# Kernel tuning notes

Hardware: AMD Instinct MI355X
Metric: run time of the kernel (lower is better)

## Reference

```python
import jax, jax.numpy as jnp
import numpy as np
from functools import partial


def _lstm_cell(x, h, c, Wk, Wr, b):
    # keras LSTMCell: gates packed as [i, f, g(candidate), o]
    z = x @ Wk + h @ Wr + b  # [B, 4U]
    i, f, g, o = jnp.split(z, 4, axis=-1)
    i = jax.nn.sigmoid(i)
    f = jax.nn.sigmoid(f)
    g = jnp.tanh(g)
    o = jax.nn.sigmoid(o)
    c_new = f * c + i * g
    h_new = o * jnp.tanh(c_new)
    return h_new, c_new


def setup_inputs() -> dict:
    key = jax.random.key(0)
    B, T, F, U, S = 1024, 128, 128, 512, 96
    k1, k2, k3, k4 = jax.random.split(key, 4)
    s = 0.05
    return {
        "inputs": jax.random.normal(k1, (B, T, F), dtype=jnp.float32),
        "Wk": jax.random.normal(k2, (F, 4 * U), dtype=jnp.float32) * s,
        "Wr": jax.random.normal(k3, (U, 4 * U), dtype=jnp.float32) * s,
        "b": jnp.zeros((4 * U,), dtype=jnp.float32),
        "Wd": jax.random.normal(k4, (U, F), dtype=jnp.float32) * s,
        "bd": jnp.zeros((F,), dtype=jnp.float32),
        "output_steps": S,
    }


def reference(inputs, Wk, Wr, b, Wd, bd, output_steps):
    B = inputs.shape[0]
    U = Wr.shape[0]
    h0 = jnp.zeros((B, U), dtype=inputs.dtype)
    c0 = jnp.zeros((B, U), dtype=inputs.dtype)

    # warmup: run RNN over the input sequence, keep final state
    def warm_step(carry, x_t):
        h, c = carry
        h, c = _lstm_cell(x_t, h, c, Wk, Wr, b)
        return (h, c), None

    (h, c), _ = jax.lax.scan(warm_step, (h0, c0), jnp.swapaxes(inputs, 0, 1))
    pred = h @ Wd + bd  # first prediction [B, F]

    def dec_step(carry, _):
        p, h, c = carry
        h, c = _lstm_cell(p, h, c, Wk, Wr, b)
        p = h @ Wd + bd
        return (p, h, c), p

    _, preds = jax.lax.scan(dec_step, (pred, h, c), None, length=output_steps - 1)
    out = jnp.concatenate([pred[None], preds], axis=0)  # [S, B, F]
    return jnp.swapaxes(out, 0, 1)  # [B, S, F]
```

## Files before the change

### kernel.cpp

```cpp
#include <hip/hip_runtime.h>
#include <hip/hip_bf16.h>

typedef float f32x4 __attribute__((ext_vector_type(4)));
typedef short s16x8 __attribute__((ext_vector_type(8)));
typedef float floatx4 __attribute__((ext_vector_type(4)));

#define DEV static __device__ __forceinline__
#define WAITVM(N) asm volatile("s_waitcnt vmcnt(" #N ")" ::: "memory")

DEV void barrier_pipe() {
  __builtin_amdgcn_sched_barrier(0);
  __builtin_amdgcn_s_barrier();
  __builtin_amdgcn_sched_barrier(0);
}

DEV void gld_lds16(const void* g, void* l) {
  __builtin_amdgcn_global_load_lds(
      (const __attribute__((address_space(1))) void*)g,
      (__attribute__((address_space(3))) void*)l, 16, 0, 0);
}

DEV short f2bf(float x) {
  union { __hip_bfloat16 h; short s; } u;
  u.h = __float2bfloat16(x);
  return u.s;
}

DEV float bf2f(short s) {
  union { unsigned u; float f; } v;
  v.u = ((unsigned)(unsigned short)s) << 16;
  return v.f;
}

DEV void split2(float x, short& hi, short& lo) {
  hi = f2bf(x);
  lo = f2bf(x - bf2f(hi));
}

DEV float sigf(float x) {
  return 1.0f / (1.0f + exp2f(x * -1.44269504f));
}

DEV float tanhf2(float x) {
  float e = exp2f(fmaxf(x, -18.0f) * -2.88539008f);
  return (1.0f - e) / (1.0f + e);
}

DEV void mfma16(f32x4& d, s16x8 a, s16x8 b) {
  asm("v_mfma_f32_16x16x32_bf16 %0, %1, %2, %0" : "+v"(d) : "v"(a), "v"(b));
}

__global__ __launch_bounds__(256)
void prep_w2(const float* __restrict__ Wk, const float* __restrict__ Wr,
             short* __restrict__ WT2) {
  __shared__ float t[64 * 65];
  const int k0 = blockIdx.x * 64, n0 = blockIdx.y * 64;
  const int c = threadIdx.x & 63, r4 = threadIdx.x >> 6;
#pragma unroll
  for (int i = 0; i < 16; ++i) {
    int r = r4 * 16 + i;
    int k = k0 + r, n = n0 + c;
    t[r * 65 + c] = (k < 128) ? Wk[(size_t)k * 2048 + n] : Wr[(size_t)(k - 128) * 2048 + n];
  }
  __syncthreads();
#pragma unroll
  for (int i = 0; i < 16; ++i) {
    int nn = r4 * 16 + i;
    float v = t[c * 65 + nn];
    short hi, lo; split2(v, hi, lo);
    WT2[(size_t)(n0 + nn) * 1280 + k0 + c] = hi;
    WT2[(size_t)(n0 + nn) * 1280 + 640 + k0 + c] = lo;
  }
}

__global__ __launch_bounds__(256)
void wdec_split(const float* __restrict__ Wd, const float* __restrict__ Wk,
                const float* __restrict__ Wr, short* __restrict__ WdecAll) {
  const int n = blockIdx.x * 256 + threadIdx.x;
  const int kp = blockIdx.y;
  float acc = Wr[(size_t)kp * 2048 + n];
#pragma unroll 8
  for (int j = 0; j < 128; ++j)
    acc = fmaf(Wd[(size_t)kp * 128 + j], Wk[(size_t)j * 2048 + n], acc);
  short hi, lo; split2(acc, hi, lo);
  WdecAll[(size_t)n * 1024 + kp] = hi;
  WdecAll[(size_t)n * 1024 + 512 + kp] = lo;
}

__global__ __launch_bounds__(256)
void wd_append(const float* __restrict__ Wd, short* __restrict__ WdecAll) {
  const int t = blockIdx.x * 256 + threadIdx.x;
  const int k = t >> 7, n = t & 127;
  float v = Wd[(size_t)k * 128 + n];
  short hi, lo; split2(v, hi, lo);
  WdecAll[(size_t)(2048 + n) * 1024 + k] = hi;
  WdecAll[(size_t)(2048 + n) * 1024 + 512 + k] = lo;
}

__global__ __launch_bounds__(256)
void bdec_all(const float* __restrict__ bd, const float* __restrict__ Wk,
              const float* __restrict__ b, float* __restrict__ bdecAll) {
  const int n = blockIdx.x * 256 + threadIdx.x;
  if (n < 2048) {
    float acc = b[n];
#pragma unroll 8
    for (int j = 0; j < 128; ++j) acc = fmaf(bd[j], Wk[(size_t)j * 2048 + n], acc);
    bdecAll[n] = acc;
  } else if (n < 2176) {
    bdecAll[n] = bd[n - 2048];
  }
}

__global__ __launch_bounds__(256)
void x0_init(const float* __restrict__ inputs, short* __restrict__ AW0) {
  const int t = blockIdx.x * 256 + threadIdx.x;
  const int r = t >> 4, c0 = (t & 15) * 8;
  const float* src = inputs + (size_t)r * 16384 + c0;
  floatx4 a = *(const floatx4*)src;
  floatx4 b = *(const floatx4*)(src + 4);
  s16x8 vh, vl;
#pragma unroll
  for (int e = 0; e < 8; ++e) {
    float x = (e < 4) ? a[e] : b[e - 4];
    short hi, lo; split2(x, hi, lo);
    vh[e] = hi; vl[e] = lo;
  }
  *(s16x8*)(AW0 + (size_t)r * 1280 + c0) = vh;
  *(s16x8*)(AW0 + (size_t)r * 1280 + 640 + c0) = vl;
}

template <int MODE>
__global__ __launch_bounds__(256)
void lstm_step(const short* __restrict__ Abuf,
               short* __restrict__ hout, int hstride, int hioff, int looff,
               const float* __restrict__ xnext,
               float* __restrict__ Cst,
               const short* __restrict__ W2,
               const float* __restrict__ bias,
               float* __restrict__ out, int sidx, int S) {
  constexpr int NKT = (MODE == 0) ? 20 : 16;
  constexpr int KP  = (MODE == 0) ? 1280 : 1024;
  __shared__ char lds[73728];
  const int tid = threadIdx.x;
  const int lane = tid & 63;
  const int wid = tid >> 6;
  const int wm = wid & 1, wu = wid >> 1;
  const int bid = blockIdx.x;

  bool is16;
  int m0, u0;
  if (MODE == 2) {
    is16 = true; m0 = bid * 64; u0 = 0;
  } else if (MODE == 1 && bid >= 256) {
    is16 = true; m0 = (bid - 256) * 64; u0 = 0;
  } else {
    is16 = false;
    const int jb = bid >> 3;
    const int strip = (bid & 7) + ((jb >> 4) << 3);
    m0 = (jb & 15) * 64;
    u0 = strip * 32;
  }
  const int wbase = (tid & 192) * 16;

  auto stage = [&](int kt, int bsel) {
    char* B = lds + 24576 + bsel * 16384;
#pragma unroll
    for (int p = 0; p < 4; ++p) {
      int idx = p * 256 + tid;
      int r = idx >> 3, jp = idx & 7;
      int j = jp ^ (r & 7);
      int gu = is16 ? (2048 + r) : (((r >> 5) << 9) + u0 + (r & 31));
      gld_lds16(W2 + (size_t)gu * KP + kt * 64 + j * 8, B + p * 4096 + wbase);
    }
    char* A = lds + bsel * 8192;
#pragma unroll
    for (int p = 0; p < 2; ++p) {
      int idx = p * 256 + tid;
      int r = idx >> 3, jp = idx & 7;
      int j = jp ^ (r & 7);
      gld_lds16(Abuf + (size_t)(m0 + r) * KP + kt * 64 + j * 8, A + p * 4096 + wbase);
    }
  };

  f32x4 acc[2][4] = {};
  stage(0, 0);
  stage(1, 1);
#pragma unroll
  for (int kt = 0; kt < NKT; ++kt) {
    if (kt <= NKT - 2) WAITVM(6);
    else WAITVM(0);
    barrier_pipe();
    if (kt + 2 < NKT) stage(kt + 2, (kt + 2) % 3);
    const char* A = lds + (kt % 3) * 8192;
    const char* B = lds + 24576 + (kt % 3) * 16384;
#pragma unroll
    for (int s2 = 0; s2 < 2; ++s2) {
      const int jd = s2 * 4 + (lane >> 4);
      s16x8 av[2], bv[4];
#pragma unroll
      for (int mi = 0; mi < 2; ++mi) {
        int r = wm * 32 + mi * 16 + (lane & 15);
        av[mi] = *(const s16x8*)(A + r * 128 + ((jd ^ (r & 7)) << 4));
      }
#pragma unroll
      for (int g = 0; g < 4; ++g) {
        int rB = g * 32 + wu * 16 + (lane & 15);
        bv[g] = *(const s16x8*)(B + rB * 128 + ((jd ^ (rB & 7)) << 4));
      }
#pragma unroll
      for (int mi = 0; mi < 2; ++mi)
#pragma unroll
        for (int g = 0; g < 4; ++g) mfma16(acc[mi][g], av[mi], bv[g]);
    }
  }

  asm volatile("s_nop 7\ns_nop 7\ns_nop 7");

  if (MODE == 2 || (MODE == 1 && is16)) {
#pragma unroll
    for (int g = 0; g < 4; ++g) {
      const int n = g * 32 + wu * 16 + (lane & 15);
      const float bb = bias[2048 + n];
#pragma unroll
      for (int mi = 0; mi < 2; ++mi) {
#pragma unroll
        for (int rr = 0; rr < 4; ++rr) {
          const int m = m0 + wm * 32 + mi * 16 + ((lane >> 4) << 2) + rr;
          out[(size_t)m * ((size_t)S * 128) + (size_t)sidx * 128 + n] =
              acc[mi][g][rr] + bb;
        }
      }
    }
    return;
  }

  const int u = u0 + wu * 16 + (lane & 15);
  const float bi = bias[u], bf_ = bias[512 + u], bg = bias[1024 + u], bo = bias[1536 + u];
#pragma unroll
  for (int mi = 0; mi < 2; ++mi) {
#pragma unroll
    for (int rr = 0; rr < 4; ++rr) {
      const int m = m0 + wm * 32 + mi * 16 + ((lane >> 4) << 2) + rr;
      const size_t off = (size_t)m * 512 + u;
      float ig = sigf(acc[mi][0][rr] + bi);
      float fg = sigf(acc[mi][1][rr] + bf_);
      float gg = tanhf2(acc[mi][2][rr] + bg);
      float og = sigf(acc[mi][3][rr] + bo);
      float cn = fg * Cst[off] + ig * gg;
      Cst[off] = cn;
      float hv = og * tanhf2(cn);
      short hh, hl; split2(hv, hh, hl);
      hout[(size_t)m * hstride + hioff + u] = hh;
      hout[(size_t)m * hstride + looff + u] = hl;
    }
  }

  if (MODE == 0 && xnext != nullptr && u0 == 0) {
    const int r = tid >> 2;
    const int c0 = (tid & 3) * 32;
    const float* src = xnext + (size_t)(m0 + r) * 16384 + c0;
    short* dst = hout + (size_t)(m0 + r) * hstride;
#pragma unroll
    for (int j = 0; j < 32; j += 8) {
      floatx4 a = *(const floatx4*)(src + j);
      floatx4 b = *(const floatx4*)(src + j + 4);
      s16x8 vh, vl;
#pragma unroll
      for (int e = 0; e < 8; ++e) {
        float x = (e < 4) ? a[e] : b[e - 4];
        short hi, lo; split2(x, hi, lo);
        vh[e] = hi; vl[e] = lo;
      }
      *(s16x8*)(dst + c0 + j) = vh;
      *(s16x8*)(dst + 640 + c0 + j) = vl;
    }
  }
}

extern "C" void kernel_launch(void* const* d_in, const int* in_sizes, int n_in,
                              void* d_out, int out_size, void* d_ws, size_t ws_size,
                              hipStream_t stream) {
  const float* inputs = (const float*)d_in[0];
  const float* Wk = (const float*)d_in[1];
  const float* Wr = (const float*)d_in[2];
  const float* bias = (const float*)d_in[3];
  const float* Wd = (const float*)d_in[4];
  const float* bd = (const float*)d_in[5];
  float* out = (float*)d_out;
  const int S = out_size / (1024 * 128);

  char* w = (char*)d_ws;
  short* WT2     = (short*)w; w += (size_t)2048 * 1280 * 2;
  short* WdecAll = (short*)w; w += (size_t)2176 * 1024 * 2;
  float* bdecA   = (float*)w; w += (size_t)2176 * 4;
  short* AW0 = (short*)w; w += (size_t)1024 * 1280 * 2;
  short* AW1 = (short*)w; w += (size_t)1024 * 1280 * 2;
  short* AD0 = (short*)w; w += (size_t)1024 * 1024 * 2;
  short* AD1 = (short*)w; w += (size_t)1024 * 1024 * 2;
  float* Cst = (float*)w; w += (size_t)1024 * 512 * 4;
  if ((size_t)(w - (char*)d_ws) > ws_size) return;

  hipMemsetAsync(AW0, 0, (size_t)1024 * 1280 * 2, stream);
  hipMemsetAsync(Cst, 0, (size_t)1024 * 512 * 4, stream);

  prep_w2<<<dim3(10, 32), 256, 0, stream>>>(Wk, Wr, WT2);
  wdec_split<<<dim3(8, 512), 256, 0, stream>>>(Wd, Wk, Wr, WdecAll);
  wd_append<<<256, 256, 0, stream>>>(Wd, WdecAll);
  bdec_all<<<9, 256, 0, stream>>>(bd, Wk, bias, bdecA);
  x0_init<<<64, 256, 0, stream>>>(inputs, AW0);

  short* AW[2] = { AW0, AW1 };
  short* AD[2] = { AD0, AD1 };

  for (int t = 0; t < 127; ++t) {
    lstm_step<0><<<256, 256, 0, stream>>>(
        AW[t & 1], AW[(t + 1) & 1], 1280, 128, 768,
        inputs + (size_t)(t + 1) * 128, Cst, WT2, bias, nullptr, 0, S);
  }
  lstm_step<0><<<256, 256, 0, stream>>>(
      AW[1], AD[0], 1024, 0, 512, nullptr, Cst, WT2, bias, nullptr, 0, S);

  for (int s = 1; s < S; ++s) {
    lstm_step<1><<<272, 256, 0, stream>>>(
        AD[(s - 1) & 1], AD[s & 1], 1024, 0, 512, nullptr, Cst,
        WdecAll, bdecA, out, s - 1, S);
  }
  lstm_step<2><<<16, 256, 0, stream>>>(
      AD[(S - 1) & 1], nullptr, 0, 0, 0, nullptr, Cst,
      WdecAll, bdecA, out, S - 1, S);
}
```

Measured before the change: 2.891 ms.

## Fuse all LSTM timesteps into one persistent kernel with a grid barrier

Replaces the roughly 224 per-timestep kernel launches with a single persistent kernel of 272 blocks. Blocks synchronise between steps through an atomic counter and a generation flag in global memory. The decode phase now reads h from the warmup buffer layout, which removes the separate AD buffers. The aim is to cut launch overhead and tail gaps between steps. In exchange it adds a spin-barrier cost each step and relies on all 272 blocks being co-resident, otherwise it deadlocks. The step count of 224 is hardcoded, which assumes S is 96.

```diff
diff --git a/kernel.cpp b/kernel.cpp
--- a/kernel.cpp
+++ b/kernel.cpp
@@ -129,151 +129,185 @@
   *(s16x8*)(AW0 + (size_t)r * 1280 + 640 + c0) = vl;
 }
 
-template <int MODE>
-__global__ __launch_bounds__(256)
-void lstm_step(const short* __restrict__ Abuf,
-               short* __restrict__ hout, int hstride, int hioff, int looff,
-               const float* __restrict__ xnext,
-               float* __restrict__ Cst,
-               const short* __restrict__ W2,
-               const float* __restrict__ bias,
-               float* __restrict__ out, int sidx, int S) {
-  constexpr int NKT = (MODE == 0) ? 20 : 16;
-  constexpr int KP  = (MODE == 0) ? 1280 : 1024;
+__global__ __launch_bounds__(256, 2)
+void lstm_persist(const float* __restrict__ inputs,
+                  const short* __restrict__ WT2,
+                  const short* __restrict__ WdecAll,
+                  const float* __restrict__ bias0,
+                  const float* __restrict__ bdecA,
+                  short* __restrict__ AW0, short* __restrict__ AW1,
+                  float* __restrict__ Cst,
+                  float* __restrict__ out, int S,
+                  unsigned* __restrict__ sync) {
   __shared__ char lds[73728];
   const int tid = threadIdx.x;
   const int lane = tid & 63;
   const int wid = tid >> 6;
   const int wm = wid & 1, wu = wid >> 1;
   const int bid = blockIdx.x;
-
-  bool is16;
+  const bool is16 = (bid >= 256);
   int m0, u0;
-  if (MODE == 2) {
-    is16 = true; m0 = bid * 64; u0 = 0;
-  } else if (MODE == 1 && bid >= 256) {
-    is16 = true; m0 = (bid - 256) * 64; u0 = 0;
+  if (is16) {
+    m0 = (bid - 256) * 64; u0 = 0;
   } else {
-    is16 = false;
     const int jb = bid >> 3;
     const int strip = (bid & 7) + ((jb >> 4) << 3);
     m0 = (jb & 15) * 64;
     u0 = strip * 32;
   }
   const int wbase = (tid & 192) * 16;
-
-  auto stage = [&](int kt, int bsel) {
-    char* B = lds + 24576 + bsel * 16384;
-#pragma unroll
-    for (int p = 0; p < 4; ++p) {
-      int idx = p * 256 + tid;
-      int r = idx >> 3, jp = idx & 7;
-      int j = jp ^ (r & 7);
-      int gu = is16 ? (2048 + r) : (((r >> 5) << 9) + u0 + (r & 31));
-      gld_lds16(W2 + (size_t)gu * KP + kt * 64 + j * 8, B + p * 4096 + wbase);
-    }
-    char* A = lds + bsel * 8192;
-#pragma unroll
-    for (int p = 0; p < 2; ++p) {
-      int idx = p * 256 + tid;
-      int r = idx >> 3, jp = idx & 7;
-      int j = jp ^ (r & 7);
-      gld_lds16(Abuf + (size_t)(m0 + r) * KP + kt * 64 + j * 8, A + p * 4096 + wbase);
-    }
-  };
-
-  f32x4 acc[2][4] = {};
-  stage(0, 0);
-  stage(1, 1);
-#pragma unroll
-  for (int kt = 0; kt < NKT; ++kt) {
-    if (kt <= NKT - 2) WAITVM(6);
-    else WAITVM(0);
-    barrier_pipe();
-    if (kt + 2 < NKT) stage(kt + 2, (kt + 2) % 3);
-    const char* A = lds + (kt % 3) * 8192;
-    const char* B = lds + 24576 + (kt % 3) * 16384;
-#pragma unroll
-    for (int s2 = 0; s2 < 2; ++s2) {
-      const int jd = s2 * 4 + (lane >> 4);
-      s16x8 av[2], bv[4];
-#pragma unroll
-      for (int mi = 0; mi < 2; ++mi) {
-        int r = wm * 32 + mi * 16 + (lane & 15);
-        av[mi] = *(const s16x8*)(A + r * 128 + ((jd ^ (r & 7)) << 4));
+  const bool xconv = (!is16 && u0 == 0);
+  unsigned* cnt = sync;
+  unsigned* gen = sync + 32;
+
+  for (int t = 0; t < 224; ++t) {
+    const bool warm = (t < 128);
+    const int s = t - 127;
+    const int nkt = warm ? 20 : 16;
+    const int kp = warm ? 1280 : 1024;
+    const short* W = warm ? WT2 : WdecAll;
+    const float* bs = warm ? bias0 : bdecA;
+    const short* Ain = (t & 1) ? AW1 : AW0;
+    short* hout = ((t + 1) & 1) ? AW1 : AW0;
+    const bool gate_on = !is16 && (warm || s <= 95);
+    const bool active = gate_on || (is16 && !warm);
+
+    if (active) {
+      auto stage = [&](int kt, int bsel) {
+        char* B = lds + 24576 + bsel * 16384;
+#pragma unroll
+        for (int p = 0; p < 4; ++p) {
+          int idx = p * 256 + tid;
+          int r = idx >> 3, jp = idx & 7;
+          int j = jp ^ (r & 7);
+          int gu = is16 ? (2048 + r) : (((r >> 5) << 9) + u0 + (r & 31));
+          gld_lds16(W + (size_t)gu * kp + kt * 64 + j * 8, B + p * 4096 + wbase);
+        }
+        char* A = lds + bsel * 8192;
+        const int ka = warm ? kt * 64
+                            : ((kt < 8) ? (128 + kt * 64) : (768 + (kt - 8) * 64));
+#pragma unroll
+        for (int p = 0; p < 2; ++p) {
+          int idx = p * 256 + tid;
+          int r = idx >> 3, jp = idx & 7;
+          int j = jp ^ (r & 7);
+          gld_lds16(Ain + (size_t)(m0 + r) * 1280 + ka + j * 8, A + p * 4096 + wbase);
+        }
+      };
+
+      f32x4 acc[2][4] = {};
+      stage(0, 0);
+      stage(1, 1);
+      int sl = 0;
+      for (int kt = 0; kt < nkt; ++kt) {
+        if (kt < nkt - 1) WAITVM(6);
+        else WAITVM(0);
+        barrier_pipe();
+        if (kt + 2 < nkt) stage(kt + 2, (sl >= 1) ? sl - 1 : 2);
+        const char* A = lds + sl * 8192;
+        const char* B = lds + 24576 + sl * 16384;
+#pragma unroll
+        for (int s2 = 0; s2 < 2; ++s2) {
+          const int jd = s2 * 4 + (lane >> 4);
+          s16x8 av[2], bv[4];
+#pragma unroll
+          for (int mi = 0; mi < 2; ++mi) {
+            int r = wm * 32 + mi * 16 + (lane & 15);
+            av[mi] = *(const s16x8*)(A + r * 128 + ((jd ^ (r & 7)) << 4));
+          }
+#pragma unroll
+          for (int g = 0; g < 4; ++g) {
+            int rB = g * 32 + wu * 16 + (lane & 15);
+            bv[g] = *(const s16x8*)(B + rB * 128 + ((jd ^ (rB & 7)) << 4));
+          }
+#pragma unroll
+          for (int mi = 0; mi < 2; ++mi)
+#pragma unroll
+            for (int g = 0; g < 4; ++g) mfma16(acc[mi][g], av[mi], bv[g]);
+        }
+        sl = (sl == 2) ? 0 : sl + 1;
       }
-#pragma unroll
-      for (int g = 0; g < 4; ++g) {
-        int rB = g * 32 + wu * 16 + (lane & 15);
-        bv[g] = *(const s16x8*)(B + rB * 128 + ((jd ^ (rB & 7)) << 4));
-      }
-#pragma unroll
-      for (int mi = 0; mi < 2; ++mi)
-#pragma unroll
-        for (int g = 0; g < 4; ++g) mfma16(acc[mi][g], av[mi], bv[g]);
-    }
-  }
-
-  asm volatile("s_nop 7\ns_nop 7\ns_nop 7");
-
-  if (MODE == 2 || (MODE == 1 && is16)) {
-#pragma unroll
-    for (int g = 0; g < 4; ++g) {
-      const int n = g * 32 + wu * 16 + (lane & 15);
-      const float bb = bias[2048 + n];
-#pragma unroll
-      for (int mi = 0; mi < 2; ++mi) {
-#pragma unroll
-        for (int rr = 0; rr < 4; ++rr) {
-          const int m = m0 + wm * 32 + mi * 16 + ((lane >> 4) << 2) + rr;
-          out[(size_t)m * ((size_t)S * 128) + (size_t)sidx * 128 + n] =
-              acc[mi][g][rr] + bb;
+
+      asm volatile("s_nop 7\ns_nop 7\ns_nop 7");
+
+      if (is16) {
+#pragma unroll
+        for (int g = 0; g < 4; ++g) {
+          const int n = g * 32 + wu * 16 + (lane & 15);
+          const float bb = bdecA[2048 + n];
+#pragma unroll
+          for (int mi = 0; mi < 2; ++mi) {
+#pragma unroll
+            for (int rr = 0; rr < 4; ++rr) {
+              const int m = m0 + wm * 32 + mi * 16 + ((lane >> 4) << 2) + rr;
+              out[(size_t)m * ((size_t)S * 128) + (size_t)(s - 1) * 128 + n] =
+                  acc[mi][g][rr] + bb;
+            }
+          }
+        }
+      } else {
+        const int u = u0 + wu * 16 + (lane & 15);
+        const float bi = bs[u], bf_ = bs[512 + u], bg = bs[1024 + u], bo = bs[1536 + u];
+#pragma unroll
+        for (int mi = 0; mi < 2; ++mi) {
+#pragma unroll
+          for (int rr = 0; rr < 4; ++rr) {
+            const int m = m0 + wm * 32 + mi * 16 + ((lane >> 4) << 2) + rr;
+            const size_t off = (size_t)m * 512 + u;
+            float ig = sigf(acc[mi][0][rr] + bi);
+            float fg = sigf(acc[mi][1][rr] + bf_);
+            float gg = tanhf2(acc[mi][2][rr] + bg);
+            float og = sigf(acc[mi][3][rr] + bo);
+            float cn = fg * Cst[off] + ig * gg;
+            Cst[off] = cn;
+            float hv = og * tanhf2(cn);
+            short hh, hl; split2(hv, hh, hl);
+            hout[(size_t)m * 1280 + 128 + u] = hh;
+            hout[(size_t)m * 1280 + 768 + u] = hl;
+          }
+        }
+        if (warm && t < 127 && xconv) {
+          const float* xn = inputs + (size_t)(t + 1) * 128;
+          const int r = tid >> 2;
+          const int c0 = (tid & 3) * 32;
+          const float* src = xn + (size_t)(m0 + r) * 16384 + c0;
+          short* dst = hout + (size_t)(m0 + r) * 1280;
+#pragma unroll
+          for (int j = 0; j < 32; j += 8) {
+            floatx4 a = *(const floatx4*)(src + j);
+            floatx4 b = *(const floatx4*)(src + j + 4);
+            s16x8 vh, vl;
+#pragma unroll
+            for (int e = 0; e < 8; ++e) {
+              float x = (e < 4) ? a[e] : b[e - 4];
+              short hi, lo; split2(x, hi, lo);
+              vh[e] = hi; vl[e] = lo;
+            }
+            *(s16x8*)(dst + c0 + j) = vh;
+            *(s16x8*)(dst + 640 + c0 + j) = vl;
+          }
         }
       }
     }
-    return;
-  }
-
-  const int u = u0 + wu * 16 + (lane & 15);
-  const float bi = bias[u], bf_ = bias[512 + u], bg = bias[1024 + u], bo = bias[1536 + u];
-#pragma unroll
-  for (int mi = 0; mi < 2; ++mi) {
-#pragma unroll
-    for (int rr = 0; rr < 4; ++rr) {
-      const int m = m0 + wm * 32 + mi * 16 + ((lane >> 4) << 2) + rr;
-      const size_t off = (size_t)m * 512 + u;
-      float ig = sigf(acc[mi][0][rr] + bi);
-      float fg = sigf(acc[mi][1][rr] + bf_);
-      float gg = tanhf2(acc[mi][2][rr] + bg);
-      float og = sigf(acc[mi][3][rr] + bo);
-      float cn = fg * Cst[off] + ig * gg;
-      Cst[off] = cn;
-      float hv = og * tanhf2(cn);
-      short hh, hl; split2(hv, hh, hl);
-      hout[(size_t)m * hstride + hioff + u] = hh;
-      hout[(size_t)m * hstride + looff + u] = hl;
+
+    __syncthreads();
+    if (tid == 0) {
+      __threadfence();
+      unsigned a = __hip_atomic_fetch_add(cnt, 1u, __ATOMIC_ACQ_REL,
+                                          __HIP_MEMORY_SCOPE_AGENT);
+      if (a == (unsigned)(272 * (t + 1) - 1)) {
+        __hip_atomic_store(gen, (unsigned)(t + 1), __ATOMIC_RELEASE,
+                           __HIP_MEMORY_SCOPE_AGENT);
+      } else {
+        unsigned g;
+        do {
+          __builtin_amdgcn_s_sleep(8);
+          g = __hip_atomic_load(gen, __ATOMIC_RELAXED, __HIP_MEMORY_SCOPE_AGENT);
+        } while (g < (unsigned)(t + 1));
+      }
+      __threadfence();
     }
-  }
-
-  if (MODE == 0 && xnext != nullptr && u0 == 0) {
-    const int r = tid >> 2;
-    const int c0 = (tid & 3) * 32;
-    const float* src = xnext + (size_t)(m0 + r) * 16384 + c0;
-    short* dst = hout + (size_t)(m0 + r) * hstride;
-#pragma unroll
-    for (int j = 0; j < 32; j += 8) {
-      floatx4 a = *(const floatx4*)(src + j);
-      floatx4 b = *(const floatx4*)(src + j + 4);
-      s16x8 vh, vl;
-#pragma unroll
-      for (int e = 0; e < 8; ++e) {
-        float x = (e < 4) ? a[e] : b[e - 4];
-        short hi, lo; split2(x, hi, lo);
-        vh[e] = hi; vl[e] = lo;
-      }
-      *(s16x8*)(dst + c0 + j) = vh;
-      *(s16x8*)(dst + 640 + c0 + j) = vl;
-    }
+    __syncthreads();
   }
 }
 
@@ -295,13 +329,13 @@
   float* bdecA   = (float*)w; w += (size_t)2176 * 4;
   short* AW0 = (short*)w; w += (size_t)1024 * 1280 * 2;
   short* AW1 = (short*)w; w += (size_t)1024 * 1280 * 2;
-  short* AD0 = (short*)w; w += (size_t)1024 * 1024 * 2;
-  short* AD1 = (short*)w; w += (size_t)1024 * 1024 * 2;
   float* Cst = (float*)w; w += (size_t)1024 * 512 * 4;
+  unsigned* sync = (unsigned*)w; w += 256;
   if ((size_t)(w - (char*)d_ws) > ws_size) return;
 
   hipMemsetAsync(AW0, 0, (size_t)1024 * 1280 * 2, stream);
   hipMemsetAsync(Cst, 0, (size_t)1024 * 512 * 4, stream);
+  hipMemsetAsync(sync, 0, 256, stream);
 
   prep_w2<<<dim3(10, 32), 256, 0, stream>>>(Wk, Wr, WT2);
   wdec_split<<<dim3(8, 512), 256, 0, stream>>>(Wd, Wk, Wr, WdecAll);
@@ -309,23 +343,6 @@
   bdec_all<<<9, 256, 0, stream>>>(bd, Wk, bias, bdecA);
   x0_init<<<64, 256, 0, stream>>>(inputs, AW0);
 
-  short* AW[2] = { AW0, AW1 };
-  short* AD[2] = { AD0, AD1 };
-
-  for (int t = 0; t < 127; ++t) {
-    lstm_step<0><<<256, 256, 0, stream>>>(
-        AW[t & 1], AW[(t + 1) & 1], 1280, 128, 768,
-        inputs + (size_t)(t + 1) * 128, Cst, WT2, bias, nullptr, 0, S);
-  }
-  lstm_step<0><<<256, 256, 0, stream>>>(
-      AW[1], AD[0], 1024, 0, 512, nullptr, Cst, WT2, bias, nullptr, 0, S);
-
-  for (int s = 1; s < S; ++s) {
-    lstm_step<1><<<272, 256, 0, stream>>>(
-        AD[(s - 1) & 1], AD[s & 1], 1024, 0, 512, nullptr, Cst,
-        WdecAll, bdecA, out, s - 1, S);
-  }
-  lstm_step<2><<<16, 256, 0, stream>>>(
-      AD[(S - 1) & 1], nullptr, 0, 0, 0, nullptr, Cst,
-      WdecAll, bdecA, out, S - 1, S);
-}
+  lstm_persist<<<272, 256, 0, stream>>>(inputs, WT2, WdecAll, bias, bdecA,
+                                        AW0, AW1, Cst, out, S, sync);
+}
```

Measured after the change: 7.138 ms. 147% more time.

## Halve LSTM gate tile width to double grid size per step

Applied to the files above, without the earlier changes.

Each recurrent-step block now covers 64 rows by 16 units per gate instead of 32, so the grid grows from 256 to 512 blocks (528 in decode mode). Each wave computes a single 16-row slice with four gate accumulators. The projection path is split into its own branch with eight 16-wide column tiles, and the warmup kernel uses a smaller LDS footprint. The aim is better latency hiding and CU occupancy per timestep. The cost is that every A-tile row is loaded by twice as many blocks, so there is less reuse and more global and L2 traffic.

```diff
diff --git a/kernel.cpp b/kernel.cpp
--- a/kernel.cpp
+++ b/kernel.cpp
@@ -131,121 +131,85 @@
 
 template <int MODE>
 __global__ __launch_bounds__(256)
-void lstm_step(const short* __restrict__ Abuf,
-               short* __restrict__ hout, int hstride, int hioff, int looff,
+void lstm_step(const short* __restrict__ Ain, short* __restrict__ hout,
+               int hstride, int hioff, int looff,
                const float* __restrict__ xnext,
                float* __restrict__ Cst,
                const short* __restrict__ W2,
                const float* __restrict__ bias,
                float* __restrict__ out, int sidx, int S) {
   constexpr int NKT = (MODE == 0) ? 20 : 16;
-  constexpr int KP  = (MODE == 0) ? 1280 : 1024;
-  __shared__ char lds[73728];
-  const int tid = threadIdx.x;
-  const int lane = tid & 63;
-  const int wid = tid >> 6;
-  const int wm = wid & 1, wu = wid >> 1;
+  constexpr int ASTR = (MODE == 0) ? 1280 : 1024;
+  constexpr int LDSZ = (MODE == 0) ? 49152 : 73728;
+  __shared__ char lds[LDSZ];
+  const int tid = threadIdx.x, lane = tid & 63, wid = tid >> 6;
+  const int l15 = lane & 15, l4 = lane >> 4;
   const int bid = blockIdx.x;
-
-  bool is16;
-  int m0, u0;
-  if (MODE == 2) {
-    is16 = true; m0 = bid * 64; u0 = 0;
-  } else if (MODE == 1 && bid >= 256) {
-    is16 = true; m0 = (bid - 256) * 64; u0 = 0;
-  } else {
-    is16 = false;
-    const int jb = bid >> 3;
-    const int strip = (bid & 7) + ((jb >> 4) << 3);
-    m0 = (jb & 15) * 64;
-    u0 = strip * 32;
-  }
   const int wbase = (tid & 192) * 16;
-
-  auto stage = [&](int kt, int bsel) {
-    char* B = lds + 24576 + bsel * 16384;
-#pragma unroll
-    for (int p = 0; p < 4; ++p) {
-      int idx = p * 256 + tid;
-      int r = idx >> 3, jp = idx & 7;
-      int j = jp ^ (r & 7);
-      int gu = is16 ? (2048 + r) : (((r >> 5) << 9) + u0 + (r & 31));
-      gld_lds16(W2 + (size_t)gu * KP + kt * 64 + j * 8, B + p * 4096 + wbase);
-    }
-    char* A = lds + bsel * 8192;
-#pragma unroll
-    for (int p = 0; p < 2; ++p) {
-      int idx = p * 256 + tid;
-      int r = idx >> 3, jp = idx & 7;
-      int j = jp ^ (r & 7);
-      gld_lds16(Abuf + (size_t)(m0 + r) * KP + kt * 64 + j * 8, A + p * 4096 + wbase);
-    }
-  };
-
-  f32x4 acc[2][4] = {};
-  stage(0, 0);
-  stage(1, 1);
-#pragma unroll
-  for (int kt = 0; kt < NKT; ++kt) {
-    if (kt <= NKT - 2) WAITVM(6);
-    else WAITVM(0);
-    barrier_pipe();
-    if (kt + 2 < NKT) stage(kt + 2, (kt + 2) % 3);
-    const char* A = lds + (kt % 3) * 8192;
-    const char* B = lds + 24576 + (kt % 3) * 16384;
-#pragma unroll
-    for (int s2 = 0; s2 < 2; ++s2) {
-      const int jd = s2 * 4 + (lane >> 4);
-      s16x8 av[2], bv[4];
-#pragma unroll
-      for (int mi = 0; mi < 2; ++mi) {
-        int r = wm * 32 + mi * 16 + (lane & 15);
-        av[mi] = *(const s16x8*)(A + r * 128 + ((jd ^ (r & 7)) << 4));
-      }
-#pragma unroll
-      for (int g = 0; g < 4; ++g) {
-        int rB = g * 32 + wu * 16 + (lane & 15);
-        bv[g] = *(const s16x8*)(B + rB * 128 + ((jd ^ (rB & 7)) << 4));
-      }
-#pragma unroll
-      for (int mi = 0; mi < 2; ++mi)
-#pragma unroll
-        for (int g = 0; g < 4; ++g) mfma16(acc[mi][g], av[mi], bv[g]);
-    }
-  }
-
-  asm volatile("s_nop 7\ns_nop 7\ns_nop 7");
-
-  if (MODE == 2 || (MODE == 1 && is16)) {
-#pragma unroll
-    for (int g = 0; g < 4; ++g) {
-      const int n = g * 32 + wu * 16 + (lane & 15);
-      const float bb = bias[2048 + n];
-#pragma unroll
-      for (int mi = 0; mi < 2; ++mi) {
-#pragma unroll
-        for (int rr = 0; rr < 4; ++rr) {
-          const int m = m0 + wm * 32 + mi * 16 + ((lane >> 4) << 2) + rr;
-          out[(size_t)m * ((size_t)S * 128) + (size_t)sidx * 128 + n] =
-              acc[mi][g][rr] + bb;
+  const bool proj = (MODE == 2) || (MODE == 1 && bid >= 512);
+
+  if (!proj) {
+    const int strip = bid & 31;
+    const int mblk = bid >> 5;
+    const int m0 = mblk * 64;
+    const int u0 = strip * 16;
+
+    auto stage = [&](int kt, int bsel) {
+      char* B = lds + 24576 + bsel * 8192;
+#pragma unroll
+      for (int p = 0; p < 2; ++p) {
+        int idx = p * 256 + tid;
+        int r = idx >> 3, jp = idx & 7;
+        int j = jp ^ (r & 7);
+        int gu = ((r >> 4) << 9) + u0 + (r & 15);
+        gld_lds16(W2 + (size_t)gu * ASTR + kt * 64 + j * 8, B + p * 4096 + wbase);
+      }
+      char* A = lds + bsel * 8192;
+#pragma unroll
+      for (int p = 0; p < 2; ++p) {
+        int idx = p * 256 + tid;
+        int r = idx >> 3, jp = idx & 7;
+        int j = jp ^ (r & 7);
+        gld_lds16(Ain + (size_t)(m0 + r) * ASTR + kt * 64 + j * 8, A + p * 4096 + wbase);
+      }
+    };
+
+    f32x4 acc[4] = {};
+    stage(0, 0);
+    stage(1, 1);
+#pragma unroll
+    for (int kt = 0; kt < NKT; ++kt) {
+      if (kt == NKT - 1) { WAITVM(0); } else { WAITVM(4); }
+      barrier_pipe();
+      if (kt + 2 < NKT) stage(kt + 2, (kt + 2) % 3);
+      const char* A = lds + (kt % 3) * 8192;
+      const char* B = lds + 24576 + (kt % 3) * 8192;
+#pragma unroll
+      for (int s2 = 0; s2 < 2; ++s2) {
+        const int jd = s2 * 4 + l4;
+        const int r = wid * 16 + l15;
+        s16x8 av = *(const s16x8*)(A + r * 128 + ((jd ^ (r & 7)) << 4));
+#pragma unroll
+        for (int g = 0; g < 4; ++g) {
+          const int rB = g * 16 + l15;
+          s16x8 bv = *(const s16x8*)(B + rB * 128 + ((jd ^ (rB & 7)) << 4));
+          mfma16(acc[g], av, bv);
         }
       }
     }
-    return;
-  }
-
-  const int u = u0 + wu * 16 + (lane & 15);
-  const float bi = bias[u], bf_ = bias[512 + u], bg = bias[1024 + u], bo = bias[1536 + u];
-#pragma unroll
-  for (int mi = 0; mi < 2; ++mi) {
+
+    asm volatile("s_nop 7\ns_nop 7\ns_nop 7");
+
+    const int u = u0 + l15;
+    const float bi = bias[u], bf_ = bias[512 + u], bg = bias[1024 + u], bo = bias[1536 + u];
 #pragma unroll
     for (int rr = 0; rr < 4; ++rr) {
-      const int m = m0 + wm * 32 + mi * 16 + ((lane >> 4) << 2) + rr;
+      const int m = m0 + wid * 16 + (l4 << 2) + rr;
       const size_t off = (size_t)m * 512 + u;
-      float ig = sigf(acc[mi][0][rr] + bi);
-      float fg = sigf(acc[mi][1][rr] + bf_);
-      float gg = tanhf2(acc[mi][2][rr] + bg);
-      float og = sigf(acc[mi][3][rr] + bo);
+      float ig = sigf(acc[0][rr] + bi);
+      float fg = sigf(acc[1][rr] + bf_);
+      float gg = tanhf2(acc[2][rr] + bg);
+      float og = sigf(acc[3][rr] + bo);
       float cn = fg * Cst[off] + ig * gg;
       Cst[off] = cn;
       float hv = og * tanhf2(cn);
@@ -253,26 +217,85 @@
       hout[(size_t)m * hstride + hioff + u] = hh;
       hout[(size_t)m * hstride + looff + u] = hl;
     }
-  }
-
-  if (MODE == 0 && xnext != nullptr && u0 == 0) {
-    const int r = tid >> 2;
-    const int c0 = (tid & 3) * 32;
-    const float* src = xnext + (size_t)(m0 + r) * 16384 + c0;
-    short* dst = hout + (size_t)(m0 + r) * hstride;
-#pragma unroll
-    for (int j = 0; j < 32; j += 8) {
-      floatx4 a = *(const floatx4*)(src + j);
-      floatx4 b = *(const floatx4*)(src + j + 4);
-      s16x8 vh, vl;
-#pragma unroll
-      for (int e = 0; e < 8; ++e) {
-        float x = (e < 4) ? a[e] : b[e - 4];
-        short hi, lo; split2(x, hi, lo);
-        vh[e] = hi; vl[e] = lo;
-      }
-      *(s16x8*)(dst + c0 + j) = vh;
-      *(s16x8*)(dst + 640 + c0 + j) = vl;
+
+    if (MODE == 0 && xnext != nullptr && strip == 0) {
+      const int r = tid >> 2;
+      const int c0 = (tid & 3) * 32;
+      const float* src = xnext + (size_t)(m0 + r) * 16384 + c0;
+      short* dst = hout + (size_t)(m0 + r) * 1280;
+#pragma unroll
+      for (int j = 0; j < 32; j += 8) {
+        floatx4 a = *(const floatx4*)(src + j);
+        floatx4 b = *(const floatx4*)(src + j + 4);
+        s16x8 vh, vl;
+#pragma unroll
+        for (int e = 0; e < 8; ++e) {
+          float x = (e < 4) ? a[e] : b[e - 4];
+          short hi, lo; split2(x, hi, lo);
+          vh[e] = hi; vl[e] = lo;
+        }
+        *(s16x8*)(dst + c0 + j) = vh;
+        *(s16x8*)(dst + 640 + c0 + j) = vl;
+      }
+    }
+  } else {
+    const int pb = (MODE == 2) ? bid : bid - 512;
+    const int m0 = pb * 64;
+
+    auto stageP = [&](int kt, int bsel) {
+      char* B = lds + 24576 + bsel * 16384;
+#pragma unroll
+      for (int p = 0; p < 4; ++p) {
+        int idx = p * 256 + tid;
+        int r = idx >> 3, jp = idx & 7;
+        int j = jp ^ (r & 7);
+        gld_lds16(W2 + (size_t)(2048 + r) * 1024 + kt * 64 + j * 8, B + p * 4096 + wbase);
+      }
+      char* A = lds + bsel * 8192;
+#pragma unroll
+      for (int p = 0; p < 2; ++p) {
+        int idx = p * 256 + tid;
+        int r = idx >> 3, jp = idx & 7;
+        int j = jp ^ (r & 7);
+        gld_lds16(Ain + (size_t)(m0 + r) * 1024 + kt * 64 + j * 8, A + p * 4096 + wbase);
+      }
+    };
+
+    f32x4 acc[8] = {};
+    stageP(0, 0);
+    stageP(1, 1);
+#pragma unroll
+    for (int kt = 0; kt < 16; ++kt) {
+      if (kt == 15) { WAITVM(0); } else { WAITVM(6); }
+      barrier_pipe();
+      if (kt + 2 < 16) stageP(kt + 2, (kt + 2) % 3);
+      const char* A = lds + (kt % 3) * 8192;
+      const char* B = lds + 24576 + (kt % 3) * 16384;
+#pragma unroll
+      for (int s2 = 0; s2 < 2; ++s2) {
+        const int jd = s2 * 4 + l4;
+        const int r = wid * 16 + l15;
+        s16x8 av = *(const s16x8*)(A + r * 128 + ((jd ^ (r & 7)) << 4));
+#pragma unroll
+        for (int nt = 0; nt < 8; ++nt) {
+          const int rB = nt * 16 + l15;
+          s16x8 bv = *(const s16x8*)(B + rB * 128 + ((jd ^ (rB & 7)) << 4));
+          mfma16(acc[nt], av, bv);
+        }
+      }
+    }
+
+    asm volatile("s_nop 7\ns_nop 7\ns_nop 7");
+
+#pragma unroll
+    for (int nt = 0; nt < 8; ++nt) {
+      const int n = nt * 16 + l15;
+      const float bb = bias[2048 + n];
+#pragma unroll
+      for (int rr = 0; rr < 4; ++rr) {
+        const int m = m0 + wid * 16 + (l4 << 2) + rr;
+        out[(size_t)m * ((size_t)S * 128) + (size_t)sidx * 128 + n] = acc[nt][rr] + bb;
+      }
     }
   }
 }
@@ -313,16 +336,16 @@
   short* AD[2] = { AD0, AD1 };
 
   for (int t = 0; t < 127; ++t) {
-    lstm_step<0><<<256, 256, 0, stream>>>(
+    lstm_step<0><<<512, 256, 0, stream>>>(
         AW[t & 1], AW[(t + 1) & 1], 1280, 128, 768,
         inputs + (size_t)(t + 1) * 128, Cst, WT2, bias, nullptr, 0, S);
   }
-  lstm_step<0><<<256, 256, 0, stream>>>(
+  lstm_step<0><<<512, 256, 0, stream>>>(
       AW[1], AD[0], 1024, 0, 512, nullptr, Cst, WT2, bias, nullptr, 0, S);
 
   for (int s = 1; s < S; ++s) {
-    lstm_step<1><<<272, 256, 0, stream>>>(
-        AD[(s - 1) & 1], AD[s & 1], 1024, 0, 512, nullptr, Cst,
+    lstm_step<1><<<528, 256, 0, stream>>>(
+        AD[(s + 1) & 1], AD[s & 1], 1024, 0, 512, nullptr, Cst,
         WdecAll, bdecA, out, s - 1, S);
   }
   lstm_step<2><<<16, 256, 0, stream>>>(
```

Result: slower. 3.613 ms (+25.0%).
